# Performance work log

Hardware: AMD Instinct MI355X
Metric: run time of the kernel (lower is better)

The kernel has to match this reference:

```python
import jax, jax.numpy as jnp
import numpy as np

H = 512
B = 64
S = 2048
NUM_LAYERS = 1


def setup_inputs() -> dict:
    key = jax.random.key(0)
    ks = jax.random.split(key, 8)
    scale = 1.0 / np.sqrt(H)
    return {
        "hidden": jax.random.normal(ks[0], (NUM_LAYERS, B, H), dtype=jnp.float32),
        "encoder_outputs": jax.random.normal(ks[1], (B, S, H), dtype=jnp.float32),
        "U_w": jax.random.uniform(ks[2], (H, H), jnp.float32, -scale, scale),
        "U_b": jax.random.uniform(ks[3], (H,), jnp.float32, -scale, scale),
        "W_w": jax.random.uniform(ks[4], (H, H), jnp.float32, -scale, scale),
        "W_b": jax.random.uniform(ks[5], (H,), jnp.float32, -scale, scale),
        "V_w": jax.random.uniform(ks[6], (1, H), jnp.float32, -scale, scale),
        "V_b": jax.random.uniform(ks[7], (1,), jnp.float32, -scale, scale),
    }


def reference(hidden, encoder_outputs, U_w, U_b, W_w, W_b, V_w, V_b):
    # hidden: [L, B, H] -> take last layer, like hidden[-1]
    h = hidden[-1]  # [B, H]
    # Uatt(h): [B, H] -> broadcast over src_len
    u = h @ U_w.T + U_b            # [B, H]
    w = jnp.einsum('bsh,kh->bsk', encoder_outputs, W_w) + W_b  # [B, S, H]
    combined = jnp.tanh(u[:, None, :] + w)                     # [B, S, H]
    energy = jnp.einsum('bsh,h->bs', combined, V_w[0]) + V_b[0]  # [B, S]
    attn = jax.nn.softmax(energy, axis=1)                       # [B, S]
    context = jnp.einsum('bs,bsh->bh', attn, encoder_outputs)   # [B, H]
    return (context, attn)
```

## Files before the change

kernel.cpp:

```cpp
#include <hip/hip_runtime.h>
#include <hip/hip_bf16.h>

#define H 512
#define B 64
#define S 2048

#define BM 128
#define BN 128
#define BK 32

typedef __bf16 bf16x8 __attribute__((ext_vector_type(8)));
typedef float f32x4 __attribute__((ext_vector_type(4)));

__device__ __forceinline__ unsigned cvt2(float x, float y) {
    union { __hip_bfloat162 h; unsigned u; } cv;
    cv.h = __float22bfloat162_rn(make_float2(x, y));
    return cv.u;
}

__device__ __forceinline__ float fast_tanh(float x) {
    float e = __expf(2.0f * x);
    float r = __builtin_amdgcn_rcpf(e + 1.0f);
    return 1.0f - 2.0f * r;
}

__global__ __launch_bounds__(256) void u_kernel(
        const float* __restrict__ hid, const float* __restrict__ Uw,
        const float* __restrict__ Ub, const float* __restrict__ Wb,
        float* __restrict__ u) {
    const int b = blockIdx.y;
    const int k = blockIdx.x * 4 + (threadIdx.x >> 6);
    const int lane = threadIdx.x & 63;
    const float4* wrow = (const float4*)(Uw + (size_t)k * H);
    const float4* hrow = (const float4*)(hid + (size_t)b * H);
    float4 w0 = wrow[lane * 2], w1 = wrow[lane * 2 + 1];
    float4 h0 = hrow[lane * 2], h1 = hrow[lane * 2 + 1];
    float acc = w0.x * h0.x + w0.y * h0.y + w0.z * h0.z + w0.w * h0.w
              + w1.x * h1.x + w1.y * h1.y + w1.z * h1.z + w1.w * h1.w;
    #pragma unroll
    for (int off = 1; off < 64; off <<= 1) acc += __shfl_xor(acc, off, 64);
    if (lane == 0) u[b * H + k] = acc + Ub[k] + Wb[k];
}

__global__ __launch_bounds__(256) void energy_kernel(
        const float* __restrict__ enc, const float* __restrict__ Ww,
        const float* __restrict__ Vw, const float* __restrict__ u,
        float* __restrict__ energy) {
    const int st = blockIdx.x;
    const int b  = blockIdx.y;
    const int s0 = st * BM;
    const int tid  = threadIdx.x;
    const int wave = tid >> 6;
    const int lane = tid & 63;
    const int wr = wave >> 1, wc = wave & 1;
    const int quad = lane >> 4, c = lane & 15;

    __shared__ unsigned short As[BM][BK];
    __shared__ unsigned short Bs[BN][BK];
    __shared__ float uS[H], vS[H];
    __shared__ float red[BM];

    #pragma unroll
    for (int i = tid; i < H; i += 256) { uS[i] = u[b * H + i]; vS[i] = Vw[i]; }

    const int srow = tid >> 3;
    const int sc4  = (tid & 7) * 4;
    const float* pA = enc + ((size_t)(b * S + s0) + srow) * H + sc4;

    float esum[4][4] = {};

    for (int kt = 0; kt < 4; ++kt) {
        const float* pB = Ww + ((size_t)(kt * BN) + srow) * H + sc4;
        f32x4 acc[4][4] = {};

        float4 pa[4], pb[4];
        #pragma unroll
        for (int i = 0; i < 4; ++i) {
            pa[i] = *(const float4*)(pA + (size_t)i * 32 * H);
            pb[i] = *(const float4*)(pB + (size_t)i * 32 * H);
        }

        for (int kk = 0; kk < H / BK; ++kk) {
            uint2 ap[4], bp[4];
            #pragma unroll
            for (int i = 0; i < 4; ++i) {
                ap[i].x = cvt2(pa[i].x, pa[i].y); ap[i].y = cvt2(pa[i].z, pa[i].w);
                bp[i].x = cvt2(pb[i].x, pb[i].y); bp[i].y = cvt2(pb[i].z, pb[i].w);
            }
            __syncthreads();
            #pragma unroll
            for (int i = 0; i < 4; ++i) {
                *(uint2*)&As[srow + i * 32][sc4] = ap[i];
                *(uint2*)&Bs[srow + i * 32][sc4] = bp[i];
            }
            __syncthreads();
            if (kk < H / BK - 1) {
                const int h0 = (kk + 1) * BK;
                #pragma unroll
                for (int i = 0; i < 4; ++i) {
                    pa[i] = *(const float4*)(pA + (size_t)i * 32 * H + h0);
                    pb[i] = *(const float4*)(pB + (size_t)i * 32 * H + h0);
                }
            }
            bf16x8 af[4], bfr[4];
            #pragma unroll
            for (int i = 0; i < 4; ++i) af[i]  = *(const bf16x8*)&As[wr * 64 + i * 16 + c][quad * 8];
            #pragma unroll
            for (int j = 0; j < 4; ++j) bfr[j] = *(const bf16x8*)&Bs[wc * 64 + j * 16 + c][quad * 8];
            #pragma unroll
            for (int i = 0; i < 4; ++i)
                #pragma unroll
                for (int j = 0; j < 4; ++j)
                    acc[i][j] = __builtin_amdgcn_mfma_f32_16x16x32_bf16(af[i], bfr[j], acc[i][j], 0, 0, 0);
        }

        #pragma unroll
        for (int i = 0; i < 4; ++i)
            #pragma unroll
            for (int j = 0; j < 4; ++j) {
                const int col = kt * BN + wc * 64 + j * 16 + c;
                const float v = vS[col], uu = uS[col];
                #pragma unroll
                for (int r = 0; r < 4; ++r)
                    esum[i][r] += v * fast_tanh(uu + acc[i][j][r]);
            }
    }

    #pragma unroll
    for (int i = 0; i < 4; ++i)
        #pragma unroll
        for (int r = 0; r < 4; ++r) {
            float e = esum[i][r];
            e += __shfl_xor(e, 1, 64);
            e += __shfl_xor(e, 2, 64);
            e += __shfl_xor(e, 4, 64);
            e += __shfl_xor(e, 8, 64);
            esum[i][r] = e;
        }
    __syncthreads();
    if (wc == 0 && c == 0) {
        #pragma unroll
        for (int i = 0; i < 4; ++i)
            #pragma unroll
            for (int r = 0; r < 4; ++r)
                red[wr * 64 + i * 16 + quad * 4 + r] = esum[i][r];
    }
    __syncthreads();
    if (wc == 1 && c == 0) {
        #pragma unroll
        for (int i = 0; i < 4; ++i)
            #pragma unroll
            for (int r = 0; r < 4; ++r) {
                const int row = wr * 64 + i * 16 + quad * 4 + r;
                energy[b * S + s0 + row] = red[row] + esum[i][r];
            }
    }
}

__global__ void softmax_kernel(const float* __restrict__ energy, float* __restrict__ attn) {
    int b = blockIdx.x;
    int t = threadIdx.x;
    const float* e = energy + b * S;
    float v[8];
    float m = -1e30f;
    #pragma unroll
    for (int i = 0; i < 8; ++i) { v[i] = e[t + i * 256]; m = fmaxf(m, v[i]); }
    #pragma unroll
    for (int off = 1; off < 64; off <<= 1) m = fmaxf(m, __shfl_xor(m, off, 64));
    __shared__ float redm[4], reds[4];
    if ((t & 63) == 0) redm[t >> 6] = m;
    __syncthreads();
    m = fmaxf(fmaxf(redm[0], redm[1]), fmaxf(redm[2], redm[3]));
    float s = 0.f;
    #pragma unroll
    for (int i = 0; i < 8; ++i) { v[i] = __expf(v[i] - m); s += v[i]; }
    #pragma unroll
    for (int off = 1; off < 64; off <<= 1) s += __shfl_xor(s, off, 64);
    if ((t & 63) == 0) reds[t >> 6] = s;
    __syncthreads();
    float inv = 1.0f / (reds[0] + reds[1] + reds[2] + reds[3]);
    #pragma unroll
    for (int i = 0; i < 8; ++i) attn[b * S + t + i * 256] = v[i] * inv;
}

#define CCHUNK 128
__global__ __launch_bounds__(256) void context_kernel(
        const float* __restrict__ enc, const float* __restrict__ attn,
        float* __restrict__ ctx) {
    int b  = blockIdx.x >> 4;
    int ch = blockIdx.x & 15;
    int t  = threadIdx.x;
    __shared__ float aS[CCHUNK];
    if (t < CCHUNK) aS[t] = attn[b * S + ch * CCHUNK + t];
    __syncthreads();
    const float* ebase = enc + ((size_t)(b * S + ch * CCHUNK)) * H + t;
    float c0 = 0.f, c1 = 0.f;
    #pragma unroll 8
    for (int s = 0; s < CCHUNK; ++s) {
        float a = aS[s];
        c0 += a * ebase[(size_t)s * H];
        c1 += a * ebase[(size_t)s * H + 256];
    }
    atomicAdd(&ctx[b * H + t], c0);
    atomicAdd(&ctx[b * H + t + 256], c1);
}

extern "C" void kernel_launch(void* const* d_in, const int* in_sizes, int n_in,
                              void* d_out, int out_size, void* d_ws, size_t ws_size,
                              hipStream_t stream) {
    (void)in_sizes; (void)n_in; (void)out_size; (void)ws_size;
    const float* hid = (const float*)d_in[0];
    const float* enc = (const float*)d_in[1];
    const float* Uw  = (const float*)d_in[2];
    const float* Ub  = (const float*)d_in[3];
    const float* Ww  = (const float*)d_in[4];
    const float* Wb  = (const float*)d_in[5];
    const float* Vw  = (const float*)d_in[6];

    float* out_ctx  = (float*)d_out;
    float* out_attn = out_ctx + B * H;
    float* energy   = (float*)d_ws;
    float* u        = energy + B * S;

    hipMemsetAsync(d_out, 0, (size_t)B * H * sizeof(float), stream);

    u_kernel<<<dim3(H / 4, B), 256, 0, stream>>>(hid, Uw, Ub, Wb, u);
    energy_kernel<<<dim3(S / BM, B), 256, 0, stream>>>(enc, Ww, Vw, u, energy);
    softmax_kernel<<<B, 256, 0, stream>>>(energy, out_attn);
    context_kernel<<<B * (S / CCHUNK), 256, 0, stream>>>(enc, out_attn, out_ctx);
}
```

Measured before the change: 546.2 us.

## Keep encoder tile in registers and stream bf16 W chunks via async LDS loads

A small kernel now converts W_w to bf16 once per call. The energy kernel holds each wave's 32 encoder rows as bf16 MFMA fragments in registers for the whole reduction. It double-buffers 32-row chunks of bf16 W into LDS using global_load_lds with an XOR swizzle. This removes the repeated fp32 loads and conversions of W and A per K-step, and the cross-wave energy reduction through LDS. In exchange it uses much more register pressure (launch bounds of 2 blocks per SM) and adds an extra kernel launch.

```diff
diff --git a/kernel.cpp b/kernel.cpp
--- a/kernel.cpp
+++ b/kernel.cpp
@@ -4,10 +4,6 @@
 #define H 512
 #define B 64
 #define S 2048
-
-#define BM 128
-#define BN 128
-#define BK 32
 
 typedef __bf16 bf16x8 __attribute__((ext_vector_type(8)));
 typedef float f32x4 __attribute__((ext_vector_type(4)));
@@ -22,6 +18,23 @@
     float e = __expf(2.0f * x);
     float r = __builtin_amdgcn_rcpf(e + 1.0f);
     return 1.0f - 2.0f * r;
+}
+
+__device__ __forceinline__ void gload_lds16(const void* g, void* l) {
+    __builtin_amdgcn_global_load_lds(
+        (const __attribute__((address_space(1))) unsigned int*)g,
+        (__attribute__((address_space(3))) unsigned int*)l, 16, 0, 0);
+}
+
+__global__ __launch_bounds__(256) void w16_kernel(const float* __restrict__ Ww,
+                                                  unsigned short* __restrict__ w16) {
+    const int i = (blockIdx.x * 256 + threadIdx.x) * 8;
+    float4 a = *(const float4*)(Ww + i);
+    float4 b = *(const float4*)(Ww + i + 4);
+    uint4 p;
+    p.x = cvt2(a.x, a.y); p.y = cvt2(a.z, a.w);
+    p.z = cvt2(b.x, b.y); p.w = cvt2(b.z, b.w);
+    *(uint4*)(w16 + i) = p;
 }
 
 __global__ __launch_bounds__(256) void u_kernel(
@@ -42,119 +55,110 @@
     if (lane == 0) u[b * H + k] = acc + Ub[k] + Wb[k];
 }
 
-__global__ __launch_bounds__(256) void energy_kernel(
-        const float* __restrict__ enc, const float* __restrict__ Ww,
+#define CN  32
+#define NCH 16
+#define CHB (CN * H * 2)
+
+__global__ __launch_bounds__(256, 2) void energy_kernel(
+        const float* __restrict__ enc, const unsigned short* __restrict__ w16,
         const float* __restrict__ Vw, const float* __restrict__ u,
         float* __restrict__ energy) {
-    const int st = blockIdx.x;
-    const int b  = blockIdx.y;
-    const int s0 = st * BM;
-    const int tid  = threadIdx.x;
-    const int wave = tid >> 6;
-    const int lane = tid & 63;
-    const int wr = wave >> 1, wc = wave & 1;
+    const int s0  = blockIdx.x * 128;
+    const int b   = blockIdx.y;
+    const int tid = threadIdx.x;
+    const int wave = tid >> 6, lane = tid & 63;
     const int quad = lane >> 4, c = lane & 15;
 
-    __shared__ unsigned short As[BM][BK];
-    __shared__ unsigned short Bs[BN][BK];
+    __shared__ unsigned char Bs[2][CHB];
     __shared__ float uS[H], vS[H];
-    __shared__ float red[BM];
-
-    #pragma unroll
+
+    #pragma unroll
+    for (int i = 0; i < 8; ++i) {
+        const int row = i * 4 + wave;
+        const int d   = (row << 10) + lane * 16;
+        gload_lds16((const unsigned char*)w16 + (d ^ ((row & 7) << 4)),
+                    &Bs[0][row << 10]);
+    }
+
     for (int i = tid; i < H; i += 256) { uS[i] = u[b * H + i]; vS[i] = Vw[i]; }
 
-    const int srow = tid >> 3;
-    const int sc4  = (tid & 7) * 4;
-    const float* pA = enc + ((size_t)(b * S + s0) + srow) * H + sc4;
-
-    float esum[4][4] = {};
-
-    for (int kt = 0; kt < 4; ++kt) {
-        const float* pB = Ww + ((size_t)(kt * BN) + srow) * H + sc4;
-        f32x4 acc[4][4] = {};
-
-        float4 pa[4], pb[4];
-        #pragma unroll
-        for (int i = 0; i < 4; ++i) {
-            pa[i] = *(const float4*)(pA + (size_t)i * 32 * H);
-            pb[i] = *(const float4*)(pB + (size_t)i * 32 * H);
-        }
-
-        for (int kk = 0; kk < H / BK; ++kk) {
-            uint2 ap[4], bp[4];
+    bf16x8 areg[2][16];
+    #pragma unroll
+    for (int g = 0; g < 2; ++g) {
+        const float* pa = enc + ((size_t)(b * S + s0 + wave * 32 + g * 16 + c)) * H + quad * 8;
+        float4 x0[16], x1[16];
+        #pragma unroll
+        for (int t = 0; t < 16; ++t) {
+            x0[t] = *(const float4*)(pa + t * 32);
+            x1[t] = *(const float4*)(pa + t * 32 + 4);
+        }
+        #pragma unroll
+        for (int t = 0; t < 16; ++t) {
+            uint4 p;
+            p.x = cvt2(x0[t].x, x0[t].y); p.y = cvt2(x0[t].z, x0[t].w);
+            p.z = cvt2(x1[t].x, x1[t].y); p.w = cvt2(x1[t].z, x1[t].w);
+            areg[g][t] = *(bf16x8*)&p;
+        }
+        __builtin_amdgcn_sched_barrier(0);
+    }
+
+    float esum[2][4] = {};
+    const int mask = (c & 7) << 4;
+
+    #pragma unroll 2
+    for (int cc = 0; cc < NCH; ++cc) {
+        const int buf = cc & 1;
+        if (cc) __syncthreads();
+        if (cc < NCH - 1) {
+            const unsigned char* src = (const unsigned char*)w16 + (cc + 1) * CHB;
             #pragma unroll
-            for (int i = 0; i < 4; ++i) {
-                ap[i].x = cvt2(pa[i].x, pa[i].y); ap[i].y = cvt2(pa[i].z, pa[i].w);
-                bp[i].x = cvt2(pb[i].x, pb[i].y); bp[i].y = cvt2(pb[i].z, pb[i].w);
+            for (int i = 0; i < 8; ++i) {
+                const int row = i * 4 + wave;
+                const int d   = (row << 10) + lane * 16;
+                gload_lds16(src + (d ^ ((row & 7) << 4)), &Bs[buf ^ 1][row << 10]);
             }
-            __syncthreads();
+            asm volatile("s_waitcnt vmcnt(8)" ::: "memory");
+        } else {
+            asm volatile("s_waitcnt vmcnt(0)" ::: "memory");
+        }
+        __syncthreads();
+
+        const unsigned char* bb = Bs[buf];
+        f32x4 acc[2][2] = {};
+        #pragma unroll
+        for (int t = 0; t < 16; ++t) {
+            const int base = t * 64 + quad * 16;
+            bf16x8 b0 = *(const bf16x8*)(bb + ((( c       << 10) + base) ^ mask));
+            bf16x8 b1 = *(const bf16x8*)(bb + ((((16 + c) << 10) + base) ^ mask));
+            acc[0][0] = __builtin_amdgcn_mfma_f32_16x16x32_bf16(areg[0][t], b0, acc[0][0], 0, 0, 0);
+            acc[1][0] = __builtin_amdgcn_mfma_f32_16x16x32_bf16(areg[1][t], b0, acc[1][0], 0, 0, 0);
+            acc[0][1] = __builtin_amdgcn_mfma_f32_16x16x32_bf16(areg[0][t], b1, acc[0][1], 0, 0, 0);
+            acc[1][1] = __builtin_amdgcn_mfma_f32_16x16x32_bf16(areg[1][t], b1, acc[1][1], 0, 0, 0);
+        }
+        #pragma unroll
+        for (int ct = 0; ct < 2; ++ct) {
+            const int col = cc * CN + ct * 16 + c;
+            const float vv = vS[col], uu = uS[col];
             #pragma unroll
-            for (int i = 0; i < 4; ++i) {
-                *(uint2*)&As[srow + i * 32][sc4] = ap[i];
-                *(uint2*)&Bs[srow + i * 32][sc4] = bp[i];
-            }
-            __syncthreads();
-            if (kk < H / BK - 1) {
-                const int h0 = (kk + 1) * BK;
-                #pragma unroll
-                for (int i = 0; i < 4; ++i) {
-                    pa[i] = *(const float4*)(pA + (size_t)i * 32 * H + h0);
-                    pb[i] = *(const float4*)(pB + (size_t)i * 32 * H + h0);
-                }
-            }
-            bf16x8 af[4], bfr[4];
-            #pragma unroll
-            for (int i = 0; i < 4; ++i) af[i]  = *(const bf16x8*)&As[wr * 64 + i * 16 + c][quad * 8];
-            #pragma unroll
-            for (int j = 0; j < 4; ++j) bfr[j] = *(const bf16x8*)&Bs[wc * 64 + j * 16 + c][quad * 8];
-            #pragma unroll
-            for (int i = 0; i < 4; ++i)
-                #pragma unroll
-                for (int j = 0; j < 4; ++j)
-                    acc[i][j] = __builtin_amdgcn_mfma_f32_16x16x32_bf16(af[i], bfr[j], acc[i][j], 0, 0, 0);
-        }
-
-        #pragma unroll
-        for (int i = 0; i < 4; ++i)
-            #pragma unroll
-            for (int j = 0; j < 4; ++j) {
-                const int col = kt * BN + wc * 64 + j * 16 + c;
-                const float v = vS[col], uu = uS[col];
+            for (int g = 0; g < 2; ++g)
                 #pragma unroll
                 for (int r = 0; r < 4; ++r)
-                    esum[i][r] += v * fast_tanh(uu + acc[i][j][r]);
-            }
-    }
-
-    #pragma unroll
-    for (int i = 0; i < 4; ++i)
+                    esum[g][r] += vv * fast_tanh(uu + acc[g][ct][r]);
+        }
+    }
+
+    #pragma unroll
+    for (int g = 0; g < 2; ++g)
         #pragma unroll
         for (int r = 0; r < 4; ++r) {
-            float e = esum[i][r];
+            float e = esum[g][r];
             e += __shfl_xor(e, 1, 64);
             e += __shfl_xor(e, 2, 64);
             e += __shfl_xor(e, 4, 64);
             e += __shfl_xor(e, 8, 64);
-            esum[i][r] = e;
-        }
-    __syncthreads();
-    if (wc == 0 && c == 0) {
-        #pragma unroll
-        for (int i = 0; i < 4; ++i)
-            #pragma unroll
-            for (int r = 0; r < 4; ++r)
-                red[wr * 64 + i * 16 + quad * 4 + r] = esum[i][r];
-    }
-    __syncthreads();
-    if (wc == 1 && c == 0) {
-        #pragma unroll
-        for (int i = 0; i < 4; ++i)
-            #pragma unroll
-            for (int r = 0; r < 4; ++r) {
-                const int row = wr * 64 + i * 16 + quad * 4 + r;
-                energy[b * S + s0 + row] = red[row] + esum[i][r];
-            }
-    }
+            if (c == 0)
+                energy[b * S + s0 + wave * 32 + g * 16 + quad * 4 + r] = e;
+        }
 }
 
 __global__ void softmax_kernel(const float* __restrict__ energy, float* __restrict__ attn) {
@@ -221,11 +225,13 @@
     float* out_attn = out_ctx + B * H;
     float* energy   = (float*)d_ws;
     float* u        = energy + B * S;
+    unsigned short* w16 = (unsigned short*)(u + B * H);
 
     hipMemsetAsync(d_out, 0, (size_t)B * H * sizeof(float), stream);
 
+    w16_kernel<<<dim3(H * H / (256 * 8)), 256, 0, stream>>>(Ww, w16);
     u_kernel<<<dim3(H / 4, B), 256, 0, stream>>>(hid, Uw, Ub, Wb, u);
-    energy_kernel<<<dim3(S / BM, B), 256, 0, stream>>>(enc, Ww, Vw, u, energy);
+    energy_kernel<<<dim3(S / 128, B), 256, 0, stream>>>(enc, w16, Vw, u, energy);
     softmax_kernel<<<B, 256, 0, stream>>>(energy, out_attn);
     context_kernel<<<B * (S / CCHUNK), 256, 0, stream>>>(enc, out_attn, out_ctx);
 }
```

Result: faster. 480.5 us (-12.0%).
